# Performance work log

Hardware: AMD Instinct MI355X
Metric: run time of the kernel (lower is better)

Reference implementation:

```python
import jax, jax.numpy as jnp
import numpy as np

NH = 8    # num_heads
HD = 64   # head_dim
EPS = 1e-6


def setup_inputs() -> dict:
    key = jax.random.key(0)
    ks = jax.random.split(key, 8)
    B, N, D = 16, 3136, 512
    x = jax.random.normal(ks[0], (B, N, D), jnp.float32)
    Wq = jax.random.normal(ks[1], (D, D), jnp.float32) * 0.02
    Wkv = jax.random.normal(ks[2], (D, 2 * D), jnp.float32) * 0.02
    pos_enc = jax.random.normal(ks[3], (1, N, D), jnp.float32) * 0.02
    # depthwise conv: fan_out = k*k*out/groups = 25
    dwc_w = jax.random.normal(ks[4], (HD, 1, 5, 5), jnp.float32) * np.sqrt(2.0 / 25.0).astype(np.float32)
    dwc_b = jnp.zeros((HD,), jnp.float32)
    Wp = jax.random.normal(ks[5], (D, D), jnp.float32) * 0.02
    bp = jnp.zeros((D,), jnp.float32)
    return {"x": x, "Wq": Wq, "Wkv": Wkv, "pos_enc": pos_enc,
            "dwc_w": dwc_w, "dwc_b": dwc_b, "Wp": Wp, "bp": bp,
            "H": 56, "W": 56}


def reference(x, Wq, Wkv, pos_enc, dwc_w, dwc_b, Wp, bp, H, W):
    B, N, D = x.shape
    # projections (qkv_bias=False)
    q = jax.nn.relu(x @ Wq)                       # ReLU feature map on q
    kv = x @ Wkv                                  # [B, N, 2D]
    k = jax.nn.relu(kv[..., :D] + pos_enc)        # pos enc added before ReLU kernel
    v = kv[..., D:]
    # split heads: b n (h c) -> b h n c
    qh = q.reshape(B, N, NH, HD).transpose(0, 2, 1, 3)
    kh = k.reshape(B, N, NH, HD).transpose(0, 2, 1, 3)
    vh = v.reshape(B, N, NH, HD).transpose(0, 2, 1, 3)
    # linear attention: normalization and KV context
    k_sum = kh.sum(axis=2)                                        # [B, NH, HD]
    d_inv = 1.0 / (jnp.einsum('bhnd,bhd->bhn', qh, k_sum) + EPS)  # [B, NH, N]
    ctx = jnp.einsum('bhmd,bhme->bhde', kh, vh)                   # [B, NH, HD, HD]
    attn = jnp.einsum('bhnd,bhde->bhne', qh, ctx) * d_inv[..., None]
    # depthwise conv positional mixing on v (N == H*W)
    fmap = vh.reshape(B * NH, H, W, HD).transpose(0, 3, 1, 2)     # [(b h), c, H, W]
    dwc = jax.lax.conv_general_dilated(
        fmap, dwc_w, window_strides=(1, 1), padding='SAME',
        feature_group_count=HD,
        dimension_numbers=('NCHW', 'OIHW', 'NCHW')) + dwc_b[None, :, None, None]
    dwc = dwc.transpose(0, 2, 3, 1).reshape(B, NH, N, HD)
    # NOTE: original torch code reshapes ((b h), n, c) -> (B, N, D) directly
    # (NOT the inverse rearrange); reproduce that exact flat reshape.
    out = (attn + dwc).reshape(B, N, D)
    return out @ Wp + bp
```

## Files before the change

### kernel.cpp

```cpp
#include <hip/hip_runtime.h>

__device__ __forceinline__ float b2f(ushort u) {
    union { float f; unsigned int i; } w; w.i = ((unsigned int)u) << 16; return w.f;
}
__device__ __forceinline__ ushort f2b(float f) {
    union { float f; unsigned int i; } w; w.f = f;
    unsigned int lsb = (w.i >> 16) & 1u;
    w.i += 0x7fffu + lsb;
    return (ushort)(w.i >> 16);
}

typedef __bf16 bf16x8 __attribute__((ext_vector_type(8)));
typedef float floatx4 __attribute__((ext_vector_type(4)));

__device__ __forceinline__ void async_copy16(ushort* lds_base, const ushort* gptr) {
    __builtin_amdgcn_global_load_lds(
        (const __attribute__((address_space(1))) unsigned int*)gptr,
        (__attribute__((address_space(3))) unsigned int*)lds_base,
        16, 0, 0);
}

#define BATCH 16
#define NTOK  3136
#define NHEAD 8
#define HDIM  64
#define HSP   56
#define MROWS (BATCH * NTOK)
#define KDIM  512

__global__ __launch_bounds__(256) void detect_dtype(const ushort* __restrict__ x,
                                                    int* __restrict__ flag)
{
    __shared__ int s;
    if (threadIdx.x == 0) s = 0;
    __syncthreads();
    int bad = 0;
    for (int i = threadIdx.x; i < 4096; i += 256) {
        int e = (x[i] >> 7) & 0xFF;
        if (e >= 0x90) bad = 1;
    }
    if (bad) s = 1;
    __syncthreads();
    if (threadIdx.x == 0) flag[0] = s;
}

__global__ __launch_bounds__(256) void convert_x(
    const void* __restrict__ x, const int* __restrict__ flag,
    ushort* __restrict__ xbf)
{
    size_t t = (size_t)blockIdx.x * 256 + threadIdx.x;
    if (flag[0]) {
        const float* xf = (const float*)x + t * 8;
        float4 f0 = *(const float4*)xf;
        float4 f1 = *(const float4*)(xf + 4);
        ushort o[8] = { f2b(f0.x), f2b(f0.y), f2b(f0.z), f2b(f0.w),
                        f2b(f1.x), f2b(f1.y), f2b(f1.z), f2b(f1.w) };
        *(uint4*)(xbf + t * 8) = *(const uint4*)o;
    } else {
        *(uint4*)(xbf + t * 8) = *((const uint4*)x + t);
    }
}

__global__ __launch_bounds__(256) void prep_weights(
    const void* __restrict__ Wq, const void* __restrict__ Wkv,
    const void* __restrict__ Wp, const int* __restrict__ flag,
    ushort* __restrict__ WqkvT, ushort* __restrict__ WpT)
{
    bool f32 = flag[0] != 0;
    int idx = blockIdx.x * 256 + threadIdx.x;
    int kk = idx & 511;
    int n  = idx >> 9;
    if (n < 1536) {
        ushort val;
        if (n < 512)
            val = f32 ? f2b(((const float*)Wq)[kk * 512 + n])
                      : ((const ushort*)Wq)[kk * 512 + n];
        else
            val = f32 ? f2b(((const float*)Wkv)[kk * 1024 + (n - 512)])
                      : ((const ushort*)Wkv)[kk * 1024 + (n - 512)];
        WqkvT[n * 512 + kk] = val;
    } else {
        int n2 = n - 1536;
        WpT[n2 * 512 + kk] = f32 ? f2b(((const float*)Wp)[kk * 512 + n2])
                                 : ((const ushort*)Wp)[kk * 512 + n2];
    }
}

__global__ __launch_bounds__(256) void prep_dwc(
    const void* __restrict__ dwc_w, const void* __restrict__ dwc_b,
    const int* __restrict__ flag, float* __restrict__ wT)
{
    bool f32 = flag[0] != 0;
    for (int i = threadIdx.x; i < 1600; i += 256) {
        int e = i / 25, tap = i % 25;
        float w = f32 ? ((const float*)dwc_w)[i] : b2f(((const ushort*)dwc_w)[i]);
        wT[tap * 64 + e] = w;
    }
    if (threadIdx.x < 64) {
        float b = f32 ? ((const float*)dwc_b)[threadIdx.x]
                      : b2f(((const ushort*)dwc_b)[threadIdx.x]);
        wT[1600 + threadIdx.x] = b;
    }
}

#define BM 128
#define BN 128
#define BK 32
__device__ __forceinline__ int swz(int r) { return (r ^ (r >> 2)) & 3; }

#define ELS_STRIDE 66

__global__ __launch_bounds__(256) void gemm_bt(
    const ushort* __restrict__ A, const ushort* __restrict__ Bt,
    int mode, const int* __restrict__ flag,
    const void* __restrict__ pos_enc, const void* __restrict__ bias,
    void* __restrict__ out0, ushort* __restrict__ out1, ushort* __restrict__ out2)
{
    __shared__ float smemf[8448];
    ushort* su = (ushort*)smemf;
    ushort* Abuf[2] = { su, su + 4096 };
    ushort* Bbuf[2] = { su + 8192, su + 12288 };

    bool f32 = flag[0] != 0;
    int tid  = threadIdx.x;

    int nb  = gridDim.x;
    int fid = blockIdx.x + blockIdx.y * nb;
    int grp = fid / (8 * nb);
    int pos = fid % (8 * nb);
    int m0  = (grp * 8 + (pos & 7)) * BM;
    int n0  = (pos >> 3) * BN;

    int wave = tid >> 6, lane = tid & 63;
    int wm = wave & 1, wn = wave >> 1;
    int mrow = lane & 15, g = lane >> 4;

    int t0 = wave * 2;
    int li0 = t0 * 64 + lane, li1 = li0 + 64;
    int r0 = li0 >> 2, s0 = (li0 & 3) ^ swz(li0 >> 2);
    int r1 = li1 >> 2, s1 = (li1 & 3) ^ swz(li1 >> 2);
    const ushort* Ag0 = A + (size_t)(m0 + r0) * KDIM + s0 * 8;
    const ushort* Ag1 = A + (size_t)(m0 + r1) * KDIM + s1 * 8;
    const ushort* Bg0 = Bt + (size_t)(n0 + r0) * KDIM + s0 * 8;
    const ushort* Bg1 = Bt + (size_t)(n0 + r1) * KDIM + s1 * 8;

    floatx4 acc[4][4];
    #pragma unroll
    for (int i = 0; i < 4; i++)
        #pragma unroll
        for (int j = 0; j < 4; j++) acc[i][j] = (floatx4)0.f;

    async_copy16(&Abuf[0][t0 * 512], Ag0);
    async_copy16(&Abuf[0][(t0 + 1) * 512], Ag1);
    async_copy16(&Bbuf[0][t0 * 512], Bg0);
    async_copy16(&Bbuf[0][(t0 + 1) * 512], Bg1);
    __syncthreads();

    #pragma unroll
    for (int it = 0; it < 16; ++it) {
        int cur = it & 1;
        if (it < 15) {
            int nk = (it + 1) * BK;
            async_copy16(&Abuf[1 - cur][t0 * 512], Ag0 + nk);
            async_copy16(&Abuf[1 - cur][(t0 + 1) * 512], Ag1 + nk);
            async_copy16(&Bbuf[1 - cur][t0 * 512], Bg0 + nk);
            async_copy16(&Bbuf[1 - cur][(t0 + 1) * 512], Bg1 + nk);
        }
        bf16x8 af[4], bfr[4];
        #pragma unroll
        for (int i = 0; i < 4; i++) {
            int r = wm * 64 + i * 16 + mrow;
            af[i] = *(const bf16x8*)&Abuf[cur][r * 32 + (g ^ swz(r)) * 8];
        }
        #pragma unroll
        for (int i = 0; i < 4; i++) {
            int r = wn * 64 + i * 16 + mrow;
            bfr[i] = *(const bf16x8*)&Bbuf[cur][r * 32 + (g ^ swz(r)) * 8];
        }
        #pragma unroll
        for (int mi = 0; mi < 4; mi++)
            #pragma unroll
            for (int ni = 0; ni < 4; ni++)
                acc[mi][ni] = __builtin_amdgcn_mfma_f32_16x16x32_bf16(
                    af[mi], bfr[ni], acc[mi][ni], 0, 0, 0);
        __syncthreads();
    }

    int m_l = tid >> 1, seg = tid & 1;
    int row = m0 + m_l;
    int b = row / NTOK;
    int n = row - b * NTOK;

    #pragma unroll
    for (int h = 0; h < 2; ++h) {
        __syncthreads();
        if (wn == h) {
            #pragma unroll
            for (int mi = 0; mi < 4; mi++) {
                int ml = wm * 64 + mi * 16 + g * 4;
                #pragma unroll
                for (int ni = 0; ni < 4; ni++)
                    #pragma unroll
                    for (int r = 0; r < 4; r++)
                        smemf[(ml + r) * ELS_STRIDE + ni * 16 + mrow] = acc[mi][ni][r];
            }
        }
        __syncthreads();
        float v[32];
        #pragma unroll
        for (int j = 0; j < 32; j++) v[j] = smemf[m_l * ELS_STRIDE + seg * 32 + j];

        int colbase = n0 + h * 64 + seg * 32;
        if (mode == 1) {
            if (f32) {
                float* o = (float*)out0 + (size_t)row * 512 + colbase;
                #pragma unroll
                for (int j = 0; j < 32; j++) {
                    float bv = ((const float*)bias)[colbase + j];
                    o[j] = v[j] + bv;
                }
            } else {
                ushort* o = (ushort*)out0 + (size_t)row * 512 + colbase;
                #pragma unroll
                for (int j4 = 0; j4 < 4; j4++) {
                    ushort t[8];
                    #pragma unroll
                    for (int j = 0; j < 8; j++) {
                        float bv = b2f(((const ushort*)bias)[colbase + j4 * 8 + j]);
                        t[j] = f2b(v[j4 * 8 + j] + bv);
                    }
                    *(uint4*)(o + j4 * 8) = *(const uint4*)t;
                }
            }
        } else {
            if (n0 < 512) {
                int head = colbase >> 6;
                int e0 = colbase & 63;
                ushort* o = (ushort*)out0 + (((size_t)b * 8 + head) * NTOK + n) * 64 + e0;
                #pragma unroll
                for (int j4 = 0; j4 < 4; j4++) {
                    ushort t[8];
                    #pragma unroll
                    for (int j = 0; j < 8; j++) t[j] = f2b(fmaxf(v[j4 * 8 + j], 0.f));
                    *(uint4*)(o + j4 * 8) = *(const uint4*)t;
                }
            } else if (n0 < 1024) {
                int d0 = colbase - 512;
                int head = d0 >> 6;
                int e0 = d0 & 63;
                ushort* o = out1 + (((size_t)b * 8 + head) * NTOK + n) * 64 + e0;
                #pragma unroll
                for (int j4 = 0; j4 < 4; j4++) {
                    ushort t[8];
                    #pragma unroll
                    for (int j = 0; j < 8; j++) {
                        float pe = f32 ? ((const float*)pos_enc)[(size_t)n * 512 + d0 + j4 * 8 + j]
                                       : b2f(((const ushort*)pos_enc)[(size_t)n * 512 + d0 + j4 * 8 + j]);
                        t[j] = f2b(fmaxf(v[j4 * 8 + j] + pe, 0.f));
                    }
                    *(uint4*)(o + j4 * 8) = *(const uint4*)t;
                }
            } else {
                int d0 = colbase - 1024;
                int head = d0 >> 6;
                int e0 = d0 & 63;
                ushort* o = out2 + (((size_t)b * 8 + head) * NTOK + n) * 64 + e0;
                #pragma unroll
                for (int j4 = 0; j4 < 4; j4++) {
                    ushort t[8];
                    #pragma unroll
                    for (int j = 0; j < 8; j++) t[j] = f2b(v[j4 * 8 + j]);
                    *(uint4*)(o + j4 * 8) = *(const uint4*)t;
                }
            }
        }
    }
}

#define SPLITS 7
#define NPER   (NTOK / SPLITS)

__global__ __launch_bounds__(256) void ctx_ksum(
    const ushort* __restrict__ kbuf, const ushort* __restrict__ vbuf,
    float* __restrict__ ctx, float* __restrict__ ksum)
{
    __shared__ ushort kT[64 * 32];
    __shared__ ushort vT[64 * 32];
    __shared__ float ks4[256];
    int bh = blockIdx.x, sp = blockIdx.y;
    int tid = threadIdx.x;
    int lane = tid & 63, wave = tid >> 6;
    int mrow = lane & 15, g = lane >> 4;
    int r = tid & 31, cblk = tid >> 5;
    size_t base = ((size_t)bh * NTOK + sp * NPER) * 64;

    floatx4 acc[4];
    #pragma unroll
    for (int c = 0; c < 4; c++) acc[c] = (floatx4)0.f;
    float kpart = 0.f;
    int kd = tid >> 2, kq = tid & 3;

    for (int nc = 0; nc < NPER; nc += 32) {
        uint4 ku = *(const uint4*)(kbuf + base + (size_t)(nc + r) * 64 + cblk * 8);
        uint4 vu = *(const uint4*)(vbuf + base + (size_t)(nc + r) * 64 + cblk * 8);
        __syncthreads();
        const ushort* kp = (const ushort*)&ku;
        const ushort* vp = (const ushort*)&vu;
        #pragma unroll
        for (int j = 0; j < 8; j++) {
            int d = cblk * 8 + j;
            int blk = (r >> 3) ^ swz(d);
            kT[d * 32 + blk * 8 + (r & 7)] = kp[j];
            vT[d * 32 + blk * 8 + (r & 7)] = vp[j];
        }
        __syncthreads();
        {
            const ushort* p = &kT[kd * 32 + kq * 8];
            #pragma unroll
            for (int j = 0; j < 8; j++) kpart += b2f(p[j]);
        }
        int dr = wave * 16 + mrow;
        bf16x8 af = *(const bf16x8*)&kT[dr * 32 + (g ^ swz(dr)) * 8];
        #pragma unroll
        for (int c = 0; c < 4; c++) {
            int er = c * 16 + mrow;
            bf16x8 bf = *(const bf16x8*)&vT[er * 32 + (g ^ swz(er)) * 8];
            acc[c] = __builtin_amdgcn_mfma_f32_16x16x32_bf16(af, bf, acc[c], 0, 0, 0);
        }
    }
    #pragma unroll
    for (int c = 0; c < 4; c++)
        #pragma unroll
        for (int rr = 0; rr < 4; rr++) {
            int d = wave * 16 + g * 4 + rr;
            int e = c * 16 + mrow;
            atomicAdd(&ctx[bh * 4096 + d * 64 + e], acc[c][rr]);
        }
    ks4[tid] = kpart;
    __syncthreads();
    if (tid < 64) {
        float s = ks4[tid * 4] + ks4[tid * 4 + 1] + ks4[tid * 4 + 2] + ks4[tid * 4 + 3];
        atomicAdd(&ksum[bh * 64 + tid], s);
    }
}

__global__ __launch_bounds__(256) void attn_kernel(
    const ushort* __restrict__ q, const float* __restrict__ ctx,
    const float* __restrict__ ksum, ushort* __restrict__ ybuf)
{
    __shared__ float smem[4352];
    ushort* ctxT = (ushort*)smem;
    float* sout = smem;
    int bh = blockIdx.x, cg = blockIdx.y;
    int tid = threadIdx.x;
    int lane = tid & 63, wave = tid >> 6;
    int mrow = lane & 15, g = lane >> 4;

    for (int i = tid; i < 640; i += 256) {
        int e = i >> 3, blk = i & 7;
        ushort tmp[8];
        #pragma unroll
        for (int j = 0; j < 8; j++) {
            int d = blk * 8 + j;
            float v = 0.f;
            if (e < 64) v = ctx[bh * 4096 + d * 64 + e];
            else if (e == 64) v = ksum[bh * 64 + d];
            tmp[j] = f2b(v);
        }
        *(uint4*)&ctxT[e * 64 + (blk ^ (e & 7)) * 8] = *(const uint4*)tmp;
    }
    __syncthreads();

    bf16x8 bfr[2][5];
    #pragma unroll
    for (int kt = 0; kt < 2; kt++)
        #pragma unroll
        for (int c = 0; c < 5; c++) {
            int e = c * 16 + mrow;
            bfr[kt][c] = *(const bf16x8*)&ctxT[e * 64 + ((kt * 4 + g) ^ (e & 7)) * 8];
        }

    int token4 = tid >> 2, seg = tid & 3;
    for (int cc = 0; cc < 7; cc++) {
        int n0 = (cg * 7 + cc) * 64;
        floatx4 acc[5];
        #pragma unroll
        for (int c = 0; c < 5; c++) acc[c] = (floatx4)0.f;
        size_t qrow = ((size_t)bh * NTOK + n0 + wave * 16 + mrow) * 64;
        #pragma unroll
        for (int kt = 0; kt < 2; kt++) {
            bf16x8 af = *(const bf16x8*)(q + qrow + kt * 32 + g * 8);
            #pragma unroll
            for (int c = 0; c < 5; c++)
                acc[c] = __builtin_amdgcn_mfma_f32_16x16x32_bf16(af, bfr[kt][c], acc[c], 0, 0, 0);
        }
        __syncthreads();
        #pragma unroll
        for (int c = 0; c < 4; c++)
            #pragma unroll
            for (int rr = 0; rr < 4; rr++)
                sout[(wave * 16 + g * 4 + rr) * 68 + c * 16 + mrow] = acc[c][rr];
        if (mrow == 0) {
            #pragma unroll
            for (int rr = 0; rr < 4; rr++)
                sout[(wave * 16 + g * 4 + rr) * 68 + 64] = acc[4][rr];
        }
        __syncthreads();
        float dinv = 1.0f / (sout[token4 * 68 + 64] + 1e-6f);
        const float* sp = &sout[token4 * 68 + seg * 16];
        ushort res[16];
        #pragma unroll
        for (int j = 0; j < 16; j++) res[j] = f2b(sp[j] * dinv);
        ushort* o = ybuf + ((size_t)bh * NTOK + n0 + token4) * 64 + seg * 16;
        *(uint4*)o = *(const uint4*)res;
        *(uint4*)(o + 8) = *(const uint4*)(res + 8);
    }
}

__global__ __launch_bounds__(256) void dwc_add(
    const ushort* __restrict__ v, const float* __restrict__ wT,
    ushort* __restrict__ ybuf)
{
    __shared__ float wls[1664];
    for (int i = threadIdx.x; i < 1664; i += 256) wls[i] = wT[i];
    __syncthreads();

    int t = blockIdx.x * 256 + threadIdx.x;
    int eg = (t & 7) * 8;
    int r = t >> 3;
    int n  = r % NTOK;
    int bh = r / NTOK;
    int y = n / HSP, x = n % HSP;

    float acc[8];
    #pragma unroll
    for (int j = 0; j < 8; j++) acc[j] = wls[1600 + eg + j];

    const ushort* vb = v + (size_t)bh * NTOK * 64 + eg;
    #pragma unroll
    for (int dy = 0; dy < 5; ++dy) {
        int yy = y + dy - 2;
        if (yy < 0 || yy >= HSP) continue;
        #pragma unroll
        for (int dx = 0; dx < 5; ++dx) {
            int xx = x + dx - 2;
            if (xx < 0 || xx >= HSP) continue;
            uint4 u = *(const uint4*)(vb + (size_t)(yy * HSP + xx) * 64);
            const ushort* up = (const ushort*)&u;
            const float* wp = &wls[(dy * 5 + dx) * 64 + eg];
            #pragma unroll
            for (int j = 0; j < 8; j++) acc[j] += wp[j] * b2f(up[j]);
        }
    }
    size_t o = (size_t)r * 64 + eg;
    uint4 yo = *(const uint4*)(ybuf + o);
    const ushort* yp = (const ushort*)&yo;
    ushort res[8];
    #pragma unroll
    for (int j = 0; j < 8; j++) res[j] = f2b(acc[j] + b2f(yp[j]));
    *(uint4*)(ybuf + o) = *(const uint4*)res;
}

extern "C" void kernel_launch(void* const* d_in, const int* in_sizes, int n_in,
                              void* d_out, int out_size, void* d_ws, size_t ws_size,
                              hipStream_t stream) {
    const void* x    = d_in[0];
    const void* Wq   = d_in[1];
    const void* Wkv  = d_in[2];
    const void* pos  = d_in[3];
    const void* dwcw = d_in[4];
    const void* dwcb = d_in[5];
    const void* Wp   = d_in[6];
    const void* bp   = d_in[7];

    char* ws = (char*)d_ws;
    const size_t SZ_BIG = 51380224;
    int*    flag   = (int*)(ws + 0);
    ushort* WqkvT  = (ushort*)(ws + 4096);
    ushort* WpT    = (ushort*)(ws + 4096 + 1572864);
    float*  wTdwc  = (float*)(ws + 2101248);
    float*  ctx    = (float*)(ws + 2107904);
    float*  ksum   = (float*)(ws + 4205056);
    ushort* qbuf   = (ushort*)(ws + 4237824);
    ushort* kbuf   = (ushort*)(ws + 4237824 + SZ_BIG);
    ushort* vbuf   = (ushort*)(ws + 4237824 + 2 * SZ_BIG);
    ushort* xbf = (ushort*)d_out;

    detect_dtype<<<1, 256, 0, stream>>>((const ushort*)x, flag);
    hipMemsetAsync(ctx, 0, 2097152 + 32768, stream);

    prep_weights<<<4096, 256, 0, stream>>>(Wq, Wkv, Wp, flag, WqkvT, WpT);
    prep_dwc<<<1, 256, 0, stream>>>(dwcw, dwcb, flag, wTdwc);
    convert_x<<<12544, 256, 0, stream>>>(x, flag, xbf);

    gemm_bt<<<dim3(1536 / BN, MROWS / BM), 256, 0, stream>>>(
        xbf, WqkvT, 0, flag, pos, nullptr, qbuf, kbuf, vbuf);

    ctx_ksum<<<dim3(128, SPLITS), 256, 0, stream>>>(kbuf, vbuf, ctx, ksum);

    attn_kernel<<<dim3(128, 7), 256, 0, stream>>>(qbuf, ctx, ksum, kbuf);

    dwc_add<<<12544, 256, 0, stream>>>(vbuf, wTdwc, kbuf);

    gemm_bt<<<dim3(512 / BN, MROWS / BM), 256, 0, stream>>>(
        kbuf, WpT, 1, flag, nullptr, bp, d_out, nullptr, nullptr);
}
```

Measured before the change: 574.1 us.

## Replace 128x128 GEMM with 256x256 tile, 8-wave, phased-prefetch MFMA kernel

Both the QKV projection and output projection GEMMs now use a 256x256 output tile with 512 threads (8 waves), a BK=64 double-buffered LDS pipeline, and XOR-swizzled layouts. Each k-step is split into four quarter phases that interleave async global-to-LDS copies with MFMA blocks, using raw barriers, explicit waitcnt and setprio. The aim is to raise arithmetic intensity per loaded byte and overlap memory with compute. The cost is 128KB of LDS per block and fewer blocks, which risks tail imbalance, especially on the 392-block output GEMM. The epilogue now stages through swizzled LDS to write 8-element vectors.

Result: faster. 538.5 us (-6.2%).

```diff
diff --git a/kernel.cpp b/kernel.cpp
--- a/kernel.cpp
+++ b/kernel.cpp
@@ -103,178 +103,222 @@
     }
 }
 
-#define BM 128
-#define BN 128
-#define BK 32
 __device__ __forceinline__ int swz(int r) { return (r ^ (r >> 2)) & 3; }
 
-#define ELS_STRIDE 66
-
-__global__ __launch_bounds__(256) void gemm_bt(
+#define VMWAIT(N) asm volatile("s_waitcnt vmcnt(" #N ")" ::: "memory")
+
+__global__ __launch_bounds__(512, 2) void gemm256_bt(
     const ushort* __restrict__ A, const ushort* __restrict__ Bt,
     int mode, const int* __restrict__ flag,
     const void* __restrict__ pos_enc, const void* __restrict__ bias,
-    void* __restrict__ out0, ushort* __restrict__ out1, ushort* __restrict__ out2)
-{
-    __shared__ float smemf[8448];
-    ushort* su = (ushort*)smemf;
-    ushort* Abuf[2] = { su, su + 4096 };
-    ushort* Bbuf[2] = { su + 8192, su + 12288 };
-
-    bool f32 = flag[0] != 0;
-    int tid  = threadIdx.x;
-
-    int nb  = gridDim.x;
-    int fid = blockIdx.x + blockIdx.y * nb;
-    int grp = fid / (8 * nb);
-    int pos = fid % (8 * nb);
-    int m0  = (grp * 8 + (pos & 7)) * BM;
-    int n0  = (pos >> 3) * BN;
-
-    int wave = tid >> 6, lane = tid & 63;
-    int wm = wave & 1, wn = wave >> 1;
-    int mrow = lane & 15, g = lane >> 4;
-
-    int t0 = wave * 2;
-    int li0 = t0 * 64 + lane, li1 = li0 + 64;
-    int r0 = li0 >> 2, s0 = (li0 & 3) ^ swz(li0 >> 2);
-    int r1 = li1 >> 2, s1 = (li1 & 3) ^ swz(li1 >> 2);
-    const ushort* Ag0 = A + (size_t)(m0 + r0) * KDIM + s0 * 8;
-    const ushort* Ag1 = A + (size_t)(m0 + r1) * KDIM + s1 * 8;
-    const ushort* Bg0 = Bt + (size_t)(n0 + r0) * KDIM + s0 * 8;
-    const ushort* Bg1 = Bt + (size_t)(n0 + r1) * KDIM + s1 * 8;
-
-    floatx4 acc[4][4];
-    #pragma unroll
-    for (int i = 0; i < 4; i++)
+    void* __restrict__ out0, ushort* __restrict__ out1, ushort* __restrict__ out2,
+    int ntn)
+{
+    __shared__ ushort smem[65536];
+
+    const bool f32 = flag[0] != 0;
+    const int tid = threadIdx.x;
+    const int lam = tid & 63;
+    const int w   = tid >> 6;
+    const int wm  = w >> 2;
+    const int wn  = w & 3;
+    const int g    = lam >> 4;
+    const int mrow = lam & 15;
+    const int m7   = mrow & 7;
+
+    const int nwg = gridDim.x;
+    const int q8  = nwg >> 3;
+    const int bid = blockIdx.x;
+    const int fid = (bid & 7) * q8 + (bid >> 3);
+    const int tm = fid / ntn, tn = fid - tm * ntn;
+    const int m0 = tm * 256, n0 = tn * 256;
+
+    const int srow = w * 16 + (lam >> 3);
+    const int scol = 8 * ((lam & 7) ^ (lam >> 3));
+    const ushort* gA0 = A  + (size_t)(m0 +       srow) * KDIM + scol;
+    const ushort* gA1 = A  + (size_t)(m0 + 128 + srow) * KDIM + scol;
+    const ushort* gB0 = Bt + (size_t)(n0 +       srow) * KDIM + scol;
+    const ushort* gB1 = Bt + (size_t)(n0 + 128 + srow) * KDIM + scol;
+
+    const int aoff = (wm * 64 + mrow) * 64;
+    const int boff = (wn * 32 + mrow) * 64;
+    const int kx0 = 8 * (g ^ m7);
+    const int kx1 = 8 * ((4 + g) ^ m7);
+
+    floatx4 acc[8][4];
+    #pragma unroll
+    for (int i = 0; i < 8; i++)
         #pragma unroll
         for (int j = 0; j < 4; j++) acc[i][j] = (floatx4)0.f;
 
-    async_copy16(&Abuf[0][t0 * 512], Ag0);
-    async_copy16(&Abuf[0][(t0 + 1) * 512], Ag1);
-    async_copy16(&Bbuf[0][t0 * 512], Bg0);
-    async_copy16(&Bbuf[0][(t0 + 1) * 512], Bg1);
-    __syncthreads();
-
-    #pragma unroll
-    for (int it = 0; it < 16; ++it) {
-        int cur = it & 1;
-        if (it < 15) {
-            int nk = (it + 1) * BK;
-            async_copy16(&Abuf[1 - cur][t0 * 512], Ag0 + nk);
-            async_copy16(&Abuf[1 - cur][(t0 + 1) * 512], Ag1 + nk);
-            async_copy16(&Bbuf[1 - cur][t0 * 512], Bg0 + nk);
-            async_copy16(&Bbuf[1 - cur][(t0 + 1) * 512], Bg1 + nk);
-        }
-        bf16x8 af[4], bfr[4];
-        #pragma unroll
-        for (int i = 0; i < 4; i++) {
-            int r = wm * 64 + i * 16 + mrow;
-            af[i] = *(const bf16x8*)&Abuf[cur][r * 32 + (g ^ swz(r)) * 8];
-        }
-        #pragma unroll
-        for (int i = 0; i < 4; i++) {
-            int r = wn * 64 + i * 16 + mrow;
-            bfr[i] = *(const bf16x8*)&Bbuf[cur][r * 32 + (g ^ swz(r)) * 8];
-        }
-        #pragma unroll
-        for (int mi = 0; mi < 4; mi++)
-            #pragma unroll
-            for (int ni = 0; ni < 4; ni++)
-                acc[mi][ni] = __builtin_amdgcn_mfma_f32_16x16x32_bf16(
-                    af[mi], bfr[ni], acc[mi][ni], 0, 0, 0);
-        __syncthreads();
-    }
-
-    int m_l = tid >> 1, seg = tid & 1;
-    int row = m0 + m_l;
-    int b = row / NTOK;
-    int n = row - b * NTOK;
-
+    bf16x8 a[4][2], bfr[2][2];
+
+#define SA(p,h) (((p)*2+(h))*8192)
+#define SB(p,h) (32768 + ((p)*2+(h))*8192)
+#define STAGE(gp, slot, koff) do { \
+    async_copy16(smem + (slot) + w*1024,       (gp) + (koff)); \
+    async_copy16(smem + (slot) + w*1024 + 512, (gp) + 4096 + (koff)); } while (0)
+
+    auto LDA_HALF = [&](int h, int p) {
+        const ushort* ab = smem + SA(p,h) + aoff;
+        #pragma unroll
+        for (int q = 0; q < 4; ++q) {
+            a[q][0] = *(const bf16x8*)(ab + q*1024 + kx0);
+            a[q][1] = *(const bf16x8*)(ab + q*1024 + kx1);
+        }
+    };
+    auto LDB_HALF = [&](int h, int p) {
+        const ushort* bb = smem + SB(p,h) + boff;
+        #pragma unroll
+        for (int nq = 0; nq < 2; ++nq) {
+            bfr[nq][0] = *(const bf16x8*)(bb + nq*1024 + kx0);
+            bfr[nq][1] = *(const bf16x8*)(bb + nq*1024 + kx1);
+        }
+    };
+
+#define PH_SYNC() do { __builtin_amdgcn_s_barrier(); \
+    asm volatile("s_waitcnt lgkmcnt(0)" ::: "memory"); \
+    __builtin_amdgcn_sched_barrier(0); } while (0)
+
+#define MFMA_QUAD(MH, NH) do { \
+    __builtin_amdgcn_s_setprio(1); \
+    _Pragma("unroll") \
+    for (int q = 0; q < 4; ++q) { \
+        _Pragma("unroll") \
+        for (int nq = 0; nq < 2; ++nq) { \
+            acc[(MH)*4+q][(NH)*2+nq] = __builtin_amdgcn_mfma_f32_16x16x32_bf16( \
+                a[q][0], bfr[nq][0], acc[(MH)*4+q][(NH)*2+nq], 0, 0, 0); \
+            acc[(MH)*4+q][(NH)*2+nq] = __builtin_amdgcn_mfma_f32_16x16x32_bf16( \
+                a[q][1], bfr[nq][1], acc[(MH)*4+q][(NH)*2+nq], 0, 0, 0); \
+        } } \
+    __builtin_amdgcn_s_setprio(0); } while (0)
+
+    STAGE(gA0, SA(0,0), 0);
+    STAGE(gB0, SB(0,0), 0);
+    STAGE(gB1, SB(0,1), 0);
+    STAGE(gA1, SA(0,1), 0);
+    VMWAIT(4);
+    __builtin_amdgcn_s_barrier();
+
+    for (int kt = 0; kt < 7; ++kt) {
+        const int p = kt & 1, np = p ^ 1;
+        const int ko = (kt + 1) * 64;
+        LDA_HALF(0, p); LDB_HALF(0, p);
+        STAGE(gA0, SA(np,0), ko);
+        VMWAIT(4);
+        PH_SYNC();
+        MFMA_QUAD(0, 0);
+        LDB_HALF(1, p);
+        STAGE(gB0, SB(np,0), ko);
+        VMWAIT(4);
+        PH_SYNC();
+        MFMA_QUAD(0, 1);
+        LDA_HALF(1, p);
+        STAGE(gB1, SB(np,1), ko);
+        PH_SYNC();
+        MFMA_QUAD(1, 1);
+        LDB_HALF(0, p);
+        STAGE(gA1, SA(np,1), ko);
+        VMWAIT(4);
+        PH_SYNC();
+        MFMA_QUAD(1, 0);
+    }
+    {
+        LDA_HALF(0, 1); LDB_HALF(0, 1);
+        VMWAIT(2);
+        PH_SYNC();
+        MFMA_QUAD(0, 0);
+        LDB_HALF(1, 1);
+        VMWAIT(0);
+        PH_SYNC();
+        MFMA_QUAD(0, 1);
+        LDA_HALF(1, 1);
+        PH_SYNC();
+        MFMA_QUAD(1, 1);
+        LDB_HALF(0, 1);
+        PH_SYNC();
+        MFMA_QUAD(1, 0);
+    }
+
+    float* lf = (float*)smem;
+    const int e0 = (lam & 7) * 8;
     #pragma unroll
     for (int h = 0; h < 2; ++h) {
         __syncthreads();
-        if (wn == h) {
-            #pragma unroll
-            for (int mi = 0; mi < 4; mi++) {
-                int ml = wm * 64 + mi * 16 + g * 4;
+        #pragma unroll
+        for (int q = 0; q < 4; ++q)
+            #pragma unroll
+            for (int ni = 0; ni < 4; ++ni)
                 #pragma unroll
-                for (int ni = 0; ni < 4; ni++)
-                    #pragma unroll
-                    for (int r = 0; r < 4; r++)
-                        smemf[(ml + r) * ELS_STRIDE + ni * 16 + mrow] = acc[mi][ni][r];
-            }
-        }
+                for (int rr = 0; rr < 4; ++rr) {
+                    int r = wm*64 + q*16 + g*4 + rr;
+                    int c = (ni>>1)*128 + wn*32 + (ni&1)*16 + mrow;
+                    lf[r*256 + (c ^ ((r&7)<<2))] = acc[h*4+q][ni][rr];
+                }
         __syncthreads();
-        float v[32];
-        #pragma unroll
-        for (int j = 0; j < 32; j++) v[j] = smemf[m_l * ELS_STRIDE + seg * 32 + j];
-
-        int colbase = n0 + h * 64 + seg * 32;
-        if (mode == 1) {
-            if (f32) {
-                float* o = (float*)out0 + (size_t)row * 512 + colbase;
-                #pragma unroll
-                for (int j = 0; j < 32; j++) {
-                    float bv = ((const float*)bias)[colbase + j];
-                    o[j] = v[j] + bv;
-                }
-            } else {
-                ushort* o = (ushort*)out0 + (size_t)row * 512 + colbase;
-                #pragma unroll
-                for (int j4 = 0; j4 < 4; j4++) {
-                    ushort t[8];
-                    #pragma unroll
-                    for (int j = 0; j < 8; j++) {
-                        float bv = b2f(((const ushort*)bias)[colbase + j4 * 8 + j]);
-                        t[j] = f2b(v[j4 * 8 + j] + bv);
+        #pragma unroll
+        for (int rh = 0; rh < 2; ++rh) {
+            const int rl = w*16 + (lam>>3) + rh*8;
+            const int rg = m0 + h*128 + rl;
+            const int bb = rg / NTOK;
+            const int nn = rg - bb*NTOK;
+            const int xr = (rl & 7) << 2;
+            const float* lrow = lf + rl*256;
+            #pragma unroll
+            for (int cb = 0; cb < 4; ++cb) {
+                const int c0 = cb*64 + e0;
+                float4 v0 = *(const float4*)(lrow + ((c0    ) ^ xr));
+                float4 v1 = *(const float4*)(lrow + ((c0 + 4) ^ xr));
+                float vv[8] = {v0.x, v0.y, v0.z, v0.w, v1.x, v1.y, v1.z, v1.w};
+                const int colg = n0 + c0;
+                if (mode == 1) {
+                    if (f32) {
+                        float ob[8];
+                        #pragma unroll
+                        for (int j = 0; j < 8; j++)
+                            ob[j] = vv[j] + ((const float*)bias)[colg + j];
+                        float* o = (float*)out0 + (size_t)rg * 512 + colg;
+                        *(float4*)o       = *(const float4*)&ob[0];
+                        *(float4*)(o + 4) = *(const float4*)&ob[4];
+                    } else {
+                        ushort t8[8];
+                        #pragma unroll
+                        for (int j = 0; j < 8; j++)
+                            t8[j] = f2b(vv[j] + b2f(((const ushort*)bias)[colg + j]));
+                        *(uint4*)((ushort*)out0 + (size_t)rg * 512 + colg) = *(const uint4*)t8;
                     }
-                    *(uint4*)(o + j4 * 8) = *(const uint4*)t;
+                } else {
+                    const int tz = colg >> 9;
+                    const size_t oadr =
+                        (((size_t)bb * 8 + ((colg >> 6) & 7)) * NTOK + nn) * 64 + (colg & 63);
+                    ushort t8[8];
+                    if (tz == 0) {
+                        #pragma unroll
+                        for (int j = 0; j < 8; j++) t8[j] = f2b(fmaxf(vv[j], 0.f));
+                        *(uint4*)((ushort*)out0 + oadr) = *(const uint4*)t8;
+                    } else if (tz == 1) {
+                        const int d0 = colg - 512;
+                        #pragma unroll
+                        for (int j = 0; j < 8; j++) {
+                            float pe = f32 ? ((const float*)pos_enc)[(size_t)nn*512 + d0 + j]
+                                           : b2f(((const ushort*)pos_enc)[(size_t)nn*512 + d0 + j]);
+                            t8[j] = f2b(fmaxf(vv[j] + pe, 0.f));
+                        }
+                        *(uint4*)(out1 + oadr) = *(const uint4*)t8;
+                    } else {
+                        #pragma unroll
+                        for (int j = 0; j < 8; j++) t8[j] = f2b(vv[j]);
+                        *(uint4*)(out2 + oadr) = *(const uint4*)t8;
+                    }
                 }
             }
-        } else {
-            if (n0 < 512) {
-                int head = colbase >> 6;
-                int e0 = colbase & 63;
-                ushort* o = (ushort*)out0 + (((size_t)b * 8 + head) * NTOK + n) * 64 + e0;
-                #pragma unroll
-                for (int j4 = 0; j4 < 4; j4++) {
-                    ushort t[8];
-                    #pragma unroll
-                    for (int j = 0; j < 8; j++) t[j] = f2b(fmaxf(v[j4 * 8 + j], 0.f));
-                    *(uint4*)(o + j4 * 8) = *(const uint4*)t;
-                }
-            } else if (n0 < 1024) {
-                int d0 = colbase - 512;
-                int head = d0 >> 6;
-                int e0 = d0 & 63;
-                ushort* o = out1 + (((size_t)b * 8 + head) * NTOK + n) * 64 + e0;
-                #pragma unroll
-                for (int j4 = 0; j4 < 4; j4++) {
-                    ushort t[8];
-                    #pragma unroll
-                    for (int j = 0; j < 8; j++) {
-                        float pe = f32 ? ((const float*)pos_enc)[(size_t)n * 512 + d0 + j4 * 8 + j]
-                                       : b2f(((const ushort*)pos_enc)[(size_t)n * 512 + d0 + j4 * 8 + j]);
-                        t[j] = f2b(fmaxf(v[j4 * 8 + j] + pe, 0.f));
-                    }
-                    *(uint4*)(o + j4 * 8) = *(const uint4*)t;
-                }
-            } else {
-                int d0 = colbase - 1024;
-                int head = d0 >> 6;
-                int e0 = d0 & 63;
-                ushort* o = out2 + (((size_t)b * 8 + head) * NTOK + n) * 64 + e0;
-                #pragma unroll
-                for (int j4 = 0; j4 < 4; j4++) {
-                    ushort t[8];
-                    #pragma unroll
-                    for (int j = 0; j < 8; j++) t[j] = f2b(v[j4 * 8 + j]);
-                    *(uint4*)(o + j4 * 8) = *(const uint4*)t;
-                }
-            }
-        }
-    }
+        }
+    }
+#undef SA
+#undef SB
+#undef STAGE
+#undef PH_SYNC
+#undef MFMA_QUAD
 }
 
 #define SPLITS 7
@@ -493,8 +537,8 @@
     prep_dwc<<<1, 256, 0, stream>>>(dwcw, dwcb, flag, wTdwc);
     convert_x<<<12544, 256, 0, stream>>>(x, flag, xbf);
 
-    gemm_bt<<<dim3(1536 / BN, MROWS / BM), 256, 0, stream>>>(
-        xbf, WqkvT, 0, flag, pos, nullptr, qbuf, kbuf, vbuf);
+    gemm256_bt<<<dim3(196 * 6), 512, 0, stream>>>(
+        xbf, WqkvT, 0, flag, pos, nullptr, qbuf, kbuf, vbuf, 6);
 
     ctx_ksum<<<dim3(128, SPLITS), 256, 0, stream>>>(kbuf, vbuf, ctx, ksum);
 
@@ -502,6 +546,6 @@
 
     dwc_add<<<12544, 256, 0, stream>>>(vbuf, wTdwc, kbuf);
 
-    gemm_bt<<<dim3(512 / BN, MROWS / BM), 256, 0, stream>>>(
-        kbuf, WpT, 1, flag, nullptr, bp, d_out, nullptr, nullptr);
-}
+    gemm256_bt<<<dim3(196 * 2), 512, 0, stream>>>(
+        kbuf, WpT, 1, flag, nullptr, bp, d_out, nullptr, nullptr, 2);
+}
```
